# Kernel optimization log

Hardware: AMD Instinct MI355X
Metric: run time of the kernel (lower is better)

The kernel has to match this reference:

```python
import jax, jax.numpy as jnp
import numpy as np

B, S, D_IN, D_H, D_OUT = 4, 2048, 512, 512, 512


def setup_inputs() -> dict:
    key = jax.random.key(0)
    ks = jax.random.split(key, 11)
    s_in = 1.0 / np.sqrt(D_IN)
    s_cat = 1.0 / np.sqrt(3 * D_H)
    return {
        "x1": jax.random.normal(ks[0], (B, S, D_IN), jnp.float32),
        "x2": jax.random.normal(ks[1], (B, S, D_IN), jnp.float32),
        "x3": jax.random.normal(ks[2], (B, S, D_IN), jnp.float32),
        "Wq": jax.random.normal(ks[3], (D_IN, D_H), jnp.float32) * s_in,
        "bq": jnp.zeros((D_H,), jnp.float32),
        "Wk": jax.random.normal(ks[4], (D_IN, D_H), jnp.float32) * s_in,
        "bk": jnp.zeros((D_H,), jnp.float32),
        "Wv": jax.random.normal(ks[5], (D_IN, D_H), jnp.float32) * s_in,
        "bv": jnp.zeros((D_H,), jnp.float32),
        "Wo": jax.random.normal(ks[6], (3 * D_H, D_OUT), jnp.float32) * s_cat,
        "bo": jnp.zeros((D_OUT,), jnp.float32),
    }


def _attn(Q, K, V):
    # Q: [B,S,H], K/V: [B,S,H] -> [B,S,H]
    scale = 1.0 / jnp.sqrt(jnp.asarray(K.shape[-1], Q.dtype))
    scores = jnp.einsum('bqh,bkh->bqk', Q, K) * scale
    w = jax.nn.softmax(scores, axis=-1)
    return jnp.einsum('bqk,bkh->bqh', w, V)


def reference(x1, x2, x3, Wq, bq, Wk, bk, Wv, bv, Wo, bo):
    Q1, Q2, Q3 = x1 @ Wq + bq, x2 @ Wq + bq, x3 @ Wq + bq
    K1, K2, K3 = x1 @ Wk + bk, x2 @ Wk + bk, x3 @ Wk + bk
    V1, V2, V3 = x1 @ Wv + bv, x2 @ Wv + bv, x3 @ Wv + bv
    fused_x1 = _attn(Q1, K2, V2) + _attn(Q1, K3, V3)
    fused_x2 = _attn(Q2, K1, V1) + _attn(Q2, K3, V3)
    fused_x3 = _attn(Q3, K1, V1) + _attn(Q3, K2, V2)
    fused = jnp.concatenate([fused_x1, fused_x2, fused_x3], axis=-1)
    return fused @ Wo + bo
```

## Files before the change

kernel.cpp:

```cpp
#include <hip/hip_runtime.h>
#include <hip/hip_bf16.h>

typedef __attribute__((ext_vector_type(4))) float  f32x4;
typedef __attribute__((ext_vector_type(8))) short  short8;
typedef __attribute__((ext_vector_type(4))) short  short4v;

#define GAS(p) ((const __attribute__((address_space(1))) void*)(p))
#define LAS(p) ((__attribute__((address_space(3))) void*)(p))

__device__ inline short bf16_of(float f) {
    union { float f; unsigned u; } v; v.f = f;
    unsigned r = v.u + 0x7FFFu + ((v.u >> 16) & 1u);
    return (short)(r >> 16);
}
__device__ inline float f_of_bf16(short h) {
    union { unsigned u; float f; } v; v.u = ((unsigned)(unsigned short)h) << 16;
    return v.f;
}

__device__ __forceinline__ void stage_tiles(const short* A, long lda,
                                            const short* B, long ldb,
                                            short* AsB, short* BsB) {
    const int tid = threadIdx.x;
    const int w = tid >> 6, l = tid & 63;
    const int r = l >> 2, ce = (l & 3) * 8;
#pragma unroll
    for (int q = 0; q < 2; ++q) {
        const int row = q * 64 + w * 16;
        __builtin_amdgcn_global_load_lds(GAS(A + (long)(row + r) * lda + ce),
                                         LAS(AsB + row * 32), 16, 0, 0);
        __builtin_amdgcn_global_load_lds(GAS(B + (long)(row + r) * ldb + ce),
                                         LAS(BsB + row * 32), 16, 0, 0);
    }
}

__device__ __forceinline__ void gemm_core(const short* A, long lda,
                                          const short* B, long ldb, int nk,
                                          short (*As)[4096], short (*Bs)[4096],
                                          f32x4 acc[4][4]) {
    const int tid = threadIdx.x;
    const int lane = tid & 63, wid = tid >> 6;
    const int wr = wid >> 1, wc = wid & 1;
    const int fr = lane & 15, fk = lane >> 4;
    const int ao = (wr * 64 + fr) * 32 + fk * 8;
    const int bo = (wc * 64 + fr) * 32 + fk * 8;

    stage_tiles(A, lda, B, ldb, As[0], Bs[0]);
    __syncthreads();
    for (int ks = 0; ks < nk; ++ks) {
        const int cur = ks & 1;
        if (ks + 1 < nk)
            stage_tiles(A + (ks + 1) * 32, lda, B + (ks + 1) * 32, ldb,
                        As[cur ^ 1], Bs[cur ^ 1]);
        short8 af[4], bf[4];
#pragma unroll
        for (int mi = 0; mi < 4; ++mi) af[mi] = *(const short8*)&As[cur][ao + mi * 512];
#pragma unroll
        for (int ni = 0; ni < 4; ++ni) bf[ni] = *(const short8*)&Bs[cur][bo + ni * 512];
#pragma unroll
        for (int mi = 0; mi < 4; ++mi)
#pragma unroll
            for (int ni = 0; ni < 4; ++ni)
                acc[mi][ni] = __builtin_amdgcn_mfma_f32_16x16x32_bf16(af[mi], bf[ni], acc[mi][ni], 0, 0, 0);
        __syncthreads();
    }
}

template<int BIAS, bool F32OUT>
__global__ __launch_bounds__(256, 2)
void gemm_bias(const short* __restrict__ A, long lda, const short* __restrict__ B, long ldb,
               void* __restrict__ Cp, long ldc, const float* __restrict__ bias, int nk) {
    __shared__ short As[2][4096], Bs[2][4096];
    const short* Ab = A + (long)blockIdx.x * 128 * lda;
    const short* Bb = B + (long)blockIdx.y * 128 * ldb;
    f32x4 acc[4][4] = {};
    gemm_core(Ab, lda, Bb, ldb, nk, As, Bs, acc);

    const int lane = threadIdx.x & 63, wid = threadIdx.x >> 6;
    const int wr = wid >> 1, wc = wid & 1, fr = lane & 15, fk = lane >> 4;
    const long r0 = (long)blockIdx.x * 128 + wr * 64 + fk * 4;
    const long c0 = (long)blockIdx.y * 128 + wc * 64 + fr;
#pragma unroll
    for (int mi = 0; mi < 4; ++mi)
#pragma unroll
        for (int ni = 0; ni < 4; ++ni) {
            const long rr = r0 + mi * 16, cc = c0 + ni * 16;
#pragma unroll
            for (int r = 0; r < 4; ++r) {
                float v = acc[mi][ni][r];
                if (BIAS == 1) v += bias[cc];
                if (BIAS == 2) v += bias[rr + r];
                if (F32OUT) ((float*)Cp)[(rr + r) * ldc + cc] = v;
                else        ((short*)Cp)[(rr + r) * ldc + cc] = bf16_of(v);
            }
        }
}

struct QKOff { long q[3], k[3], s[3], l[3]; };

__global__ __launch_bounds__(256, 2)
void qk_exp(const short* __restrict__ Q, const short* __restrict__ K,
            short* __restrict__ Sc, float* __restrict__ L, QKOff o, float kscale) {
    __shared__ short As[2][4096], Bs[2][4096];
    const int p = blockIdx.z >> 2, b = blockIdx.z & 3;
    const short* Ab = Q + o.q[p] + ((long)b * 2048 + (long)blockIdx.x * 128) * 512;
    const short* Bb = K + o.k[p] + ((long)b * 2048 + (long)blockIdx.y * 128) * 512;
    f32x4 acc[4][4] = {};
    gemm_core(Ab, 512, Bb, 512, 16, As, Bs, acc);

    short* Cb = Sc + o.s[p] + (long)b * 2048 * 2048;
    float* lb = L + o.l[p] + (long)b * 2048;
    const int lane = threadIdx.x & 63, wid = threadIdx.x >> 6;
    const int wr = wid >> 1, wc = wid & 1, fr = lane & 15, fk = lane >> 4;
    const int r0 = blockIdx.x * 128 + wr * 64 + fk * 4;
    const int c0 = blockIdx.y * 128 + wc * 64 + fr;

#pragma unroll
    for (int mi = 0; mi < 4; ++mi)
#pragma unroll
        for (int ni = 0; ni < 4; ++ni)
#pragma unroll
            for (int r = 0; r < 4; ++r)
                acc[mi][ni][r] = exp2f(acc[mi][ni][r] * kscale);

#pragma unroll
    for (int mi = 0; mi < 4; ++mi)
#pragma unroll
        for (int r = 0; r < 4; ++r) {
            float s = acc[mi][0][r] + acc[mi][1][r] + acc[mi][2][r] + acc[mi][3][r];
            s += __shfl_xor(s, 1); s += __shfl_xor(s, 2);
            s += __shfl_xor(s, 4); s += __shfl_xor(s, 8);
            if (fr == 0) atomicAdd(&lb[r0 + mi * 16 + r], s);
        }

#pragma unroll
    for (int mi = 0; mi < 4; ++mi)
#pragma unroll
        for (int ni = 0; ni < 4; ++ni)
#pragma unroll
            for (int r = 0; r < 4; ++r)
                Cb[(long)(r0 + mi * 16 + r) * 2048 + (c0 + ni * 16)] = bf16_of(acc[mi][ni][r]);
}

struct PVOff { long s[3], v[3], c[3], l[3]; int accf[3]; };

__global__ __launch_bounds__(256, 2)
void pv_div(const short* __restrict__ Sc, const short* __restrict__ VT,
            short* __restrict__ F, const float* __restrict__ L, PVOff o) {
    __shared__ short As[2][4096], Bs[2][4096];
    const int p = blockIdx.z >> 2, b = blockIdx.z & 3;
    const short* Ab = Sc + o.s[p] + ((long)b * 2048 + (long)blockIdx.x * 128) * 2048;
    const short* Bb = VT + o.v[p] + (long)b * 2048 + (long)blockIdx.y * 128 * 24576;
    f32x4 acc[4][4] = {};
    gemm_core(Ab, 2048, Bb, 24576, 64, As, Bs, acc);

    const int lane = threadIdx.x & 63, wid = threadIdx.x >> 6;
    const int wr = wid >> 1, wc = wid & 1, fr = lane & 15, fk = lane >> 4;
    const int r0loc = blockIdx.x * 128 + wr * 64 + fk * 4;
    const long rg0 = (long)b * 2048 + r0loc;
    const int c0 = blockIdx.y * 128 + wc * 64 + fr;
    const float* lb = L + o.l[p] + (long)b * 2048;
    short* Cb = F + o.c[p];

    float linv[4][4];
#pragma unroll
    for (int mi = 0; mi < 4; ++mi)
#pragma unroll
        for (int r = 0; r < 4; ++r) linv[mi][r] = 1.0f / lb[r0loc + mi * 16 + r];

    const int af = o.accf[p];
#pragma unroll
    for (int mi = 0; mi < 4; ++mi)
#pragma unroll
        for (int ni = 0; ni < 4; ++ni)
#pragma unroll
            for (int r = 0; r < 4; ++r) {
                const long idx = (rg0 + mi * 16 + r) * 1536 + (c0 + ni * 16);
                float v = acc[mi][ni][r] * linv[mi][r];
                if (af) v += f_of_bf16(Cb[idx]);
                Cb[idx] = bf16_of(v);
            }
}

__global__ __launch_bounds__(256)
void xconv(const float* __restrict__ x0, const float* __restrict__ x1,
           const float* __restrict__ x2, short* __restrict__ xb) {
    const float* s = blockIdx.z == 0 ? x0 : (blockIdx.z == 1 ? x1 : x2);
    const long i = ((long)blockIdx.x * 256 + threadIdx.x) * 8;
    f32x4 a = *(const f32x4*)(s + i), c = *(const f32x4*)(s + i + 4);
    short8 v;
    v[0] = bf16_of(a.x); v[1] = bf16_of(a.y); v[2] = bf16_of(a.z); v[3] = bf16_of(a.w);
    v[4] = bf16_of(c.x); v[5] = bf16_of(c.y); v[6] = bf16_of(c.z); v[7] = bf16_of(c.w);
    *(short8*)(xb + (long)blockIdx.z * 8192 * 512 + i) = v;
}

__global__ __launch_bounds__(256)
void transpose_to_bf16(const float* __restrict__ src, short* __restrict__ dst,
                       int rows, int cols) {
    __shared__ float t[32][33];
    const int lx = threadIdx.x & 31, ly = threadIdx.x >> 5;
    const int r0 = blockIdx.x * 32, c0 = blockIdx.y * 32;
#pragma unroll
    for (int p = 0; p < 4; ++p)
        t[ly + 8 * p][lx] = src[(long)(r0 + ly + 8 * p) * cols + (c0 + lx)];
    __syncthreads();
#pragma unroll
    for (int p = 0; p < 4; ++p)
        dst[(long)(c0 + ly + 8 * p) * rows + (r0 + lx)] = bf16_of(t[lx][ly + 8 * p]);
}

#define LDP 40
template<bool F32> struct StageRegs;
template<> struct StageRegs<true>  { f32x4 v[4]; };
template<> struct StageRegs<false> { short8 v[2]; };

template<bool F32>
__device__ inline void stage_load(const void* base, long ld, int tid, StageRegs<F32>& r) {
    if constexpr (F32) {
        const float* p = (const float*)base;
        const int row = tid >> 3, c = (tid & 7) * 4;
#pragma unroll
        for (int i = 0; i < 4; ++i)
            r.v[i] = *(const f32x4*)(p + (long)(row + 32 * i) * ld + c);
    } else {
        const short* p = (const short*)base;
        const int row = tid >> 2, c = (tid & 3) * 8;
#pragma unroll
        for (int i = 0; i < 2; ++i)
            r.v[i] = *(const short8*)(p + (long)(row + 64 * i) * ld + c);
    }
}
template<bool F32>
__device__ inline void stage_commit(short* lds, int tid, const StageRegs<F32>& r) {
    if constexpr (F32) {
        const int row = tid >> 3, c = (tid & 7) * 4;
#pragma unroll
        for (int i = 0; i < 4; ++i) {
            short4v h;
            h.x = bf16_of(r.v[i].x); h.y = bf16_of(r.v[i].y);
            h.z = bf16_of(r.v[i].z); h.w = bf16_of(r.v[i].w);
            *(short4v*)&lds[(row + 32 * i) * LDP + c] = h;
        }
    } else {
        const int row = tid >> 2, c = (tid & 3) * 8;
#pragma unroll
        for (int i = 0; i < 2; ++i)
            *(short8*)&lds[(row + 64 * i) * LDP + c] = r.v[i];
    }
}

template<bool AF32, bool BF32, int BIAS>
__global__ __launch_bounds__(256, 2)
void gemm_bt_f32(const void* __restrict__ Ap, const void* __restrict__ Bp,
                 short* __restrict__ Cp, const float* __restrict__ bias,
                 int K, long lda, long ldb, long ldc) {
    __shared__ short As[2][128 * LDP];
    __shared__ short Bs[2][128 * LDP];
    const int tid = threadIdx.x;
    const char* A = (const char*)Ap + (long)blockIdx.x * 128 * lda * (AF32 ? 4 : 2);
    const char* B = (const char*)Bp + (long)blockIdx.y * 128 * ldb * (BF32 ? 4 : 2);

    StageRegs<AF32> ra; StageRegs<BF32> rb;
    stage_load<AF32>(A, lda, tid, ra);
    stage_load<BF32>(B, ldb, tid, rb);
    stage_commit<AF32>(As[0], tid, ra);
    stage_commit<BF32>(Bs[0], tid, rb);
    __syncthreads();

    f32x4 acc[4][4] = {};
    const int lane = tid & 63, wid = tid >> 6;
    const int wr = wid >> 1, wc = wid & 1;
    const int fr = lane & 15, fk = lane >> 4;
    const int aoff = (wr * 64 + fr) * LDP + fk * 8;
    const int boff = (wc * 64 + fr) * LDP + fk * 8;

    const int nk = K / 32;
    for (int ks = 0; ks < nk; ++ks) {
        const int cur = ks & 1;
        if (ks + 1 < nk) {
            stage_load<AF32>(A + (long)(ks + 1) * 32 * (AF32 ? 4 : 2), lda, tid, ra);
            stage_load<BF32>(B + (long)(ks + 1) * 32 * (BF32 ? 4 : 2), ldb, tid, rb);
        }
        short8 af[4], bfr[4];
#pragma unroll
        for (int mi = 0; mi < 4; ++mi) af[mi] = *(const short8*)&As[cur][aoff + mi * 16 * LDP];
#pragma unroll
        for (int ni = 0; ni < 4; ++ni) bfr[ni] = *(const short8*)&Bs[cur][boff + ni * 16 * LDP];
#pragma unroll
        for (int mi = 0; mi < 4; ++mi)
#pragma unroll
            for (int ni = 0; ni < 4; ++ni)
                acc[mi][ni] = __builtin_amdgcn_mfma_f32_16x16x32_bf16(af[mi], bfr[ni], acc[mi][ni], 0, 0, 0);
        if (ks + 1 < nk) {
            stage_commit<AF32>(As[cur ^ 1], tid, ra);
            stage_commit<BF32>(Bs[cur ^ 1], tid, rb);
        }
        __syncthreads();
    }

    const long crow0 = (long)blockIdx.x * 128 + wr * 64 + fk * 4;
    const long ccol0 = (long)blockIdx.y * 128 + wc * 64 + fr;
#pragma unroll
    for (int mi = 0; mi < 4; ++mi)
#pragma unroll
        for (int ni = 0; ni < 4; ++ni) {
            const long rr = crow0 + mi * 16, cc = ccol0 + ni * 16;
#pragma unroll
            for (int r = 0; r < 4; ++r) {
                float v = acc[mi][ni][r];
                if (BIAS == 1) v += bias[cc];
                if (BIAS == 2) v += bias[rr + r];
                Cp[(rr + r) * ldc + cc] = bf16_of(v);
            }
        }
}

extern "C" void kernel_launch(void* const* d_in, const int* in_sizes, int n_in,
                              void* d_out, int out_size, void* d_ws, size_t ws_size,
                              hipStream_t stream) {
    const float* x[3] = { (const float*)d_in[0], (const float*)d_in[1], (const float*)d_in[2] };
    const float* Wq = (const float*)d_in[3]; const float* bq = (const float*)d_in[4];
    const float* Wk = (const float*)d_in[5]; const float* bk = (const float*)d_in[6];
    const float* Wv = (const float*)d_in[7]; const float* bv = (const float*)d_in[8];
    const float* Wo = (const float*)d_in[9]; const float* bo = (const float*)d_in[10];

    const long TOK = 8192;
    const long T3 = 3 * TOK;

    char* ws = (char*)d_ws;
    size_t off = 0;
    auto alloc = [&](size_t bytes) -> void* {
        void* pp = ws + off;
        off += (bytes + 255) & ~(size_t)255;
        return pp;
    };

    short* WqT = (short*)alloc(512L * 512 * 2);
    short* WkT = (short*)alloc(512L * 512 * 2);
    short* WvT = (short*)alloc(512L * 512 * 2);
    short* WoT = (short*)alloc(512L * 1536 * 2);
    short* Qb  = (short*)alloc(T3 * 512 * 2);
    short* Kb  = (short*)alloc(T3 * 512 * 2);
    short* VT  = (short*)alloc(512L * T3 * 2);
    short* fused = (short*)alloc(TOK * 1536 * 2);
    float* l   = (float*)alloc(6L * 4 * 2048 * 4);

    const size_t base = off;
    const size_t SCB = 4L * 2048 * 2048 * 2;
    const size_t XB  = T3 * 512 * 2;

    int nlive; bool use_xb;
    if      (ws_size >= base + XB + 3 * SCB) { nlive = 3; use_xb = true;  }
    else if (ws_size >= base + XB + SCB)     { nlive = 1; use_xb = true;  }
    else                                     { nlive = 1; use_xb = false; }
    short* xb     = use_xb ? (short*)alloc(XB) : nullptr;
    short* scores = (short*)alloc((size_t)nlive * SCB);

    const dim3 tb(256);

    hipMemsetAsync(l, 0, 6L * 4 * 2048 * 4, stream);

    transpose_to_bf16<<<dim3(16, 16), tb, 0, stream>>>(Wq, WqT, 512, 512);
    transpose_to_bf16<<<dim3(16, 16), tb, 0, stream>>>(Wk, WkT, 512, 512);
    transpose_to_bf16<<<dim3(16, 16), tb, 0, stream>>>(Wv, WvT, 512, 512);
    transpose_to_bf16<<<dim3(48, 16), tb, 0, stream>>>(Wo, WoT, 1536, 512);

    if (use_xb) {
        xconv<<<dim3(2048, 1, 3), tb, 0, stream>>>(x[0], x[1], x[2], xb);
        gemm_bias<1, false><<<dim3(192, 4), tb, 0, stream>>>(xb, 512, WqT, 512, Qb, 512, bq, 16);
        gemm_bias<1, false><<<dim3(192, 4), tb, 0, stream>>>(xb, 512, WkT, 512, Kb, 512, bk, 16);
        gemm_bias<2, false><<<dim3(4, 192), tb, 0, stream>>>(WvT, 512, xb, 512, VT, T3, bv, 16);
    } else {
        for (int i = 0; i < 3; ++i) {
            gemm_bt_f32<true, false, 1><<<dim3(64, 4), tb, 0, stream>>>(
                x[i], WqT, Qb + (long)i * TOK * 512, bq, 512, 512, 512, 512);
            gemm_bt_f32<true, false, 1><<<dim3(64, 4), tb, 0, stream>>>(
                x[i], WkT, Kb + (long)i * TOK * 512, bk, 512, 512, 512, 512);
            gemm_bt_f32<false, true, 2><<<dim3(4, 64), tb, 0, stream>>>(
                WvT, x[i], VT + (long)i * TOK, bv, 512, 512, 512, T3);
        }
    }

    const int imap[6] = {0, 1, 2, 0, 1, 2};
    const int jmap[6] = {1, 0, 0, 2, 2, 1};
    const int accf[6] = {0, 0, 0, 1, 1, 1};
    const float kscale = 0.04419417382415922f * 1.4426950408889634f;

    for (int g = 0; g < 6; g += nlive) {
        QKOff qo{}; PVOff po{};
        for (int pl = 0; pl < nlive; ++pl) {
            const int gp = g + pl;
            qo.q[pl] = (long)imap[gp] * TOK * 512;
            qo.k[pl] = (long)jmap[gp] * TOK * 512;
            qo.s[pl] = (long)pl * 4 * 2048 * 2048;
            qo.l[pl] = (long)gp * 4 * 2048;
            po.s[pl] = qo.s[pl];
            po.v[pl] = (long)jmap[gp] * TOK;
            po.c[pl] = (long)imap[gp] * 512;
            po.l[pl] = qo.l[pl];
            po.accf[pl] = accf[gp];
        }
        qk_exp<<<dim3(16, 16, 4 * nlive), tb, 0, stream>>>(Qb, Kb, scores, l, qo, kscale);
        pv_div<<<dim3(16, 4, 4 * nlive), tb, 0, stream>>>(scores, VT, fused, l, po);
    }

    gemm_bias<1, true><<<dim3(64, 4), tb, 0, stream>>>(fused, 1536, WoT, 1536, d_out, 512, bo, 48);
}
```

Measured before the change: 460.4 us.

## Use K=64 swizzled LDS tiles, LDS-bounced stores, deterministic row sums, split fused output

The GEMM core now stages 64-wide K tiles into XOR-swizzled LDS, which halves the number of loop iterations and barriers and avoids bank conflicts. Epilogues write bf16 results through an LDS bounce buffer so global stores are 16-byte coalesced. Softmax row sums move from atomics to per-block partials followed by a small reduction kernel. The second attention term goes to a separate fused buffer, so the read-modify-write in pv_div is gone and the sum happens in the output GEMM instead. This costs more workspace, an extra output GEMM pass, and doubled LDS per block, which may hurt occupancy.

```diff
diff --git a/kernel.cpp b/kernel.cpp
--- a/kernel.cpp
+++ b/kernel.cpp
@@ -3,7 +3,6 @@
 
 typedef __attribute__((ext_vector_type(4))) float  f32x4;
 typedef __attribute__((ext_vector_type(8))) short  short8;
-typedef __attribute__((ext_vector_type(4))) short  short4v;
 
 #define GAS(p) ((const __attribute__((address_space(1))) void*)(p))
 #define LAS(p) ((__attribute__((address_space(3))) void*)(p))
@@ -18,63 +17,126 @@
     return v.f;
 }
 
-__device__ __forceinline__ void stage_tiles(const short* A, long lda,
-                                            const short* B, long ldb,
-                                            short* AsB, short* BsB) {
+__device__ __forceinline__ void stage64(const short* A, long lda,
+                                        const short* B, long ldb,
+                                        short* As, short* Bs) {
     const int tid = threadIdx.x;
     const int w = tid >> 6, l = tid & 63;
-    const int r = l >> 2, ce = (l & 3) * 8;
-#pragma unroll
-    for (int q = 0; q < 2; ++q) {
-        const int row = q * 64 + w * 16;
-        __builtin_amdgcn_global_load_lds(GAS(A + (long)(row + r) * lda + ce),
-                                         LAS(AsB + row * 32), 16, 0, 0);
-        __builtin_amdgcn_global_load_lds(GAS(B + (long)(row + r) * ldb + ce),
-                                         LAS(BsB + row * 32), 16, 0, 0);
-    }
-}
-
-__device__ __forceinline__ void gemm_core(const short* A, long lda,
-                                          const short* B, long ldb, int nk,
-                                          short (*As)[4096], short (*Bs)[4096],
-                                          f32x4 acc[4][4]) {
+    const int r = l >> 3;
+    const int scol = ((l & 7) ^ r) * 8;
+#pragma unroll
+    for (int q = 0; q < 4; ++q) {
+        const int rowb = q * 32 + w * 8;
+        __builtin_amdgcn_global_load_lds(GAS(A + (long)(rowb + r) * lda + scol),
+                                         LAS(As + rowb * 64), 16, 0, 0);
+        __builtin_amdgcn_global_load_lds(GAS(B + (long)(rowb + r) * ldb + scol),
+                                         LAS(Bs + rowb * 64), 16, 0, 0);
+    }
+}
+
+__device__ __forceinline__ void gemm_core64(const short* A, long lda,
+                                            const short* B, long ldb, int nk,
+                                            short* sA, short* sB,
+                                            f32x4 acc[4][4]) {
     const int tid = threadIdx.x;
     const int lane = tid & 63, wid = tid >> 6;
     const int wr = wid >> 1, wc = wid & 1;
     const int fr = lane & 15, fk = lane >> 4;
-    const int ao = (wr * 64 + fr) * 32 + fk * 8;
-    const int bo = (wc * 64 + fr) * 32 + fk * 8;
-
-    stage_tiles(A, lda, B, ldb, As[0], Bs[0]);
+    const int swz = (fr & 7) << 4;
+    const int abase = (wr * 64 + fr) * 128 + fk * 16;
+    const int bbase = (wc * 64 + fr) * 128 + fk * 16;
+
+    stage64(A, lda, B, ldb, sA, sB);
     __syncthreads();
     for (int ks = 0; ks < nk; ++ks) {
         const int cur = ks & 1;
         if (ks + 1 < nk)
-            stage_tiles(A + (ks + 1) * 32, lda, B + (ks + 1) * 32, ldb,
-                        As[cur ^ 1], Bs[cur ^ 1]);
-        short8 af[4], bf[4];
-#pragma unroll
-        for (int mi = 0; mi < 4; ++mi) af[mi] = *(const short8*)&As[cur][ao + mi * 512];
-#pragma unroll
-        for (int ni = 0; ni < 4; ++ni) bf[ni] = *(const short8*)&Bs[cur][bo + ni * 512];
-#pragma unroll
-        for (int mi = 0; mi < 4; ++mi)
+            stage64(A + (ks + 1) * 64, lda, B + (ks + 1) * 64, ldb,
+                    sA + (cur ^ 1) * 8192, sB + (cur ^ 1) * 8192);
+        const char* pa = (const char*)(sA + cur * 8192);
+        const char* pb = (const char*)(sB + cur * 8192);
+        short8 af[2][4], bf[2][4];
+#pragma unroll
+        for (int kk = 0; kk < 2; ++kk) {
+#pragma unroll
+            for (int mi = 0; mi < 4; ++mi)
+                af[kk][mi] = *(const short8*)(pa + (((abase + kk * 64) ^ swz) + mi * 2048));
 #pragma unroll
             for (int ni = 0; ni < 4; ++ni)
-                acc[mi][ni] = __builtin_amdgcn_mfma_f32_16x16x32_bf16(af[mi], bf[ni], acc[mi][ni], 0, 0, 0);
+                bf[kk][ni] = *(const short8*)(pb + (((bbase + kk * 64) ^ swz) + ni * 2048));
+        }
+#pragma unroll
+        for (int kk = 0; kk < 2; ++kk)
+#pragma unroll
+            for (int mi = 0; mi < 4; ++mi)
+#pragma unroll
+                for (int ni = 0; ni < 4; ++ni)
+                    acc[mi][ni] = __builtin_amdgcn_mfma_f32_16x16x32_bf16(af[kk][mi], bf[kk][ni], acc[mi][ni], 0, 0, 0);
         __syncthreads();
     }
 }
 
-template<int BIAS, bool F32OUT>
+__device__ __forceinline__ void bounce_store(short* Pb, const short vals[4][4][4],
+                                             short* C, long ldc) {
+    const int tid = threadIdx.x, lane = tid & 63, wid = tid >> 6;
+    const int wr = wid >> 1, wc = wid & 1, fr = lane & 15, fk = lane >> 4;
+#pragma unroll
+    for (int mi = 0; mi < 4; ++mi)
+#pragma unroll
+        for (int ni = 0; ni < 4; ++ni)
+#pragma unroll
+            for (int r = 0; r < 4; ++r) {
+                const int row = wr * 64 + mi * 16 + fk * 4 + r;
+                const int col = wc * 64 + ni * 16 + fr;
+                Pb[row * 128 + (col ^ ((row & 7) << 3))] = vals[mi][ni][r];
+            }
+    __syncthreads();
+#pragma unroll
+    for (int i = 0; i < 8; ++i) {
+        const int row = i * 16 + (tid >> 4);
+        const int ch = tid & 15;
+        short8 v = *(const short8*)&Pb[row * 128 + ((ch * 8) ^ ((row & 7) << 3))];
+        *(short8*)&C[(long)row * ldc + ch * 8] = v;
+    }
+}
+
+template<int BIAS>
 __global__ __launch_bounds__(256, 2)
-void gemm_bias(const short* __restrict__ A, long lda, const short* __restrict__ B, long ldb,
-               void* __restrict__ Cp, long ldc, const float* __restrict__ bias, int nk) {
-    __shared__ short As[2][4096], Bs[2][4096];
+void gemm_bias16(const short* __restrict__ A, long lda, const short* __restrict__ B, long ldb,
+                 short* __restrict__ C, long ldc, const float* __restrict__ bias, int nk) {
+    __shared__ short sA[2 * 8192], sB[2 * 8192];
     const short* Ab = A + (long)blockIdx.x * 128 * lda;
     const short* Bb = B + (long)blockIdx.y * 128 * ldb;
     f32x4 acc[4][4] = {};
-    gemm_core(Ab, lda, Bb, ldb, nk, As, Bs, acc);
+    gemm_core64(Ab, lda, Bb, ldb, nk, sA, sB, acc);
+
+    const int lane = threadIdx.x & 63, wid = threadIdx.x >> 6;
+    const int wr = wid >> 1, wc = wid & 1, fr = lane & 15, fk = lane >> 4;
+    const long r0 = (long)blockIdx.x * 128, c0 = (long)blockIdx.y * 128;
+    short vals[4][4][4];
+#pragma unroll
+    for (int mi = 0; mi < 4; ++mi)
+#pragma unroll
+        for (int ni = 0; ni < 4; ++ni)
+#pragma unroll
+            for (int r = 0; r < 4; ++r) {
+                float v = acc[mi][ni][r];
+                if (BIAS == 1) v += bias[c0 + wc * 64 + ni * 16 + fr];
+                if (BIAS == 2) v += bias[r0 + wr * 64 + mi * 16 + fk * 4 + r];
+                vals[mi][ni][r] = bf16_of(v);
+            }
+    bounce_store(sA, vals, C + r0 * ldc + c0, ldc);
+}
+
+template<bool ACC>
+__global__ __launch_bounds__(256, 2)
+void gemm_f32(const short* __restrict__ A, long lda, const short* __restrict__ B, long ldb,
+              float* __restrict__ C, long ldc, const float* __restrict__ bias, int nk) {
+    __shared__ short sA[2 * 8192], sB[2 * 8192];
+    const short* Ab = A + (long)blockIdx.x * 128 * lda;
+    const short* Bb = B + (long)blockIdx.y * 128 * ldb;
+    f32x4 acc[4][4] = {};
+    gemm_core64(Ab, lda, Bb, ldb, nk, sA, sB, acc);
 
     const int lane = threadIdx.x & 63, wid = threadIdx.x >> 6;
     const int wr = wid >> 1, wc = wid & 1, fr = lane & 15, fk = lane >> 4;
@@ -88,32 +150,30 @@
 #pragma unroll
             for (int r = 0; r < 4; ++r) {
                 float v = acc[mi][ni][r];
-                if (BIAS == 1) v += bias[cc];
-                if (BIAS == 2) v += bias[rr + r];
-                if (F32OUT) ((float*)Cp)[(rr + r) * ldc + cc] = v;
-                else        ((short*)Cp)[(rr + r) * ldc + cc] = bf16_of(v);
+                if (!ACC) v += bias[cc];
+                const long idx = (rr + r) * ldc + cc;
+                if (ACC) v += C[idx];
+                C[idx] = v;
             }
         }
 }
 
-struct QKOff { long q[3], k[3], s[3], l[3]; };
+struct Off6 { long a[6], b[6]; };
 
 __global__ __launch_bounds__(256, 2)
 void qk_exp(const short* __restrict__ Q, const short* __restrict__ K,
-            short* __restrict__ Sc, float* __restrict__ L, QKOff o, float kscale) {
-    __shared__ short As[2][4096], Bs[2][4096];
-    const int p = blockIdx.z >> 2, b = blockIdx.z & 3;
-    const short* Ab = Q + o.q[p] + ((long)b * 2048 + (long)blockIdx.x * 128) * 512;
-    const short* Bb = K + o.k[p] + ((long)b * 2048 + (long)blockIdx.y * 128) * 512;
+            short* __restrict__ Sc, float* __restrict__ lpart,
+            Off6 o, int z0, float kscale) {
+    __shared__ short sA[2 * 8192], sB[2 * 8192];
+    const int slice = z0 + blockIdx.z;
+    const int gp = slice >> 2, b = slice & 3;
+    const short* Ab = Q + o.a[gp] + ((long)b * 2048 + (long)blockIdx.x * 128) * 512;
+    const short* Bb = K + o.b[gp] + ((long)b * 2048 + (long)blockIdx.y * 128) * 512;
     f32x4 acc[4][4] = {};
-    gemm_core(Ab, 512, Bb, 512, 16, As, Bs, acc);
-
-    short* Cb = Sc + o.s[p] + (long)b * 2048 * 2048;
-    float* lb = L + o.l[p] + (long)b * 2048;
-    const int lane = threadIdx.x & 63, wid = threadIdx.x >> 6;
-    const int wr = wid >> 1, wc = wid & 1, fr = lane & 15, fk = lane >> 4;
-    const int r0 = blockIdx.x * 128 + wr * 64 + fk * 4;
-    const int c0 = blockIdx.y * 128 + wc * 64 + fr;
+    gemm_core64(Ab, 512, Bb, 512, 8, sA, sB, acc);
+
+    const int tid = threadIdx.x, lane = tid & 63, wid = tid >> 6;
+    const int wr = wid >> 1, wc = wid & 1, fr = lane & 15, fk = lane >> 4;
 
 #pragma unroll
     for (int mi = 0; mi < 4; ++mi)
@@ -130,56 +190,72 @@
             float s = acc[mi][0][r] + acc[mi][1][r] + acc[mi][2][r] + acc[mi][3][r];
             s += __shfl_xor(s, 1); s += __shfl_xor(s, 2);
             s += __shfl_xor(s, 4); s += __shfl_xor(s, 8);
-            if (fr == 0) atomicAdd(&lb[r0 + mi * 16 + r], s);
+            if (fr == 0)
+                lpart[((long)slice * 32 + blockIdx.y * 2 + wc) * 2048 +
+                      (long)blockIdx.x * 128 + wr * 64 + mi * 16 + fk * 4 + r] = s;
         }
 
+    short vals[4][4][4];
 #pragma unroll
     for (int mi = 0; mi < 4; ++mi)
 #pragma unroll
         for (int ni = 0; ni < 4; ++ni)
 #pragma unroll
             for (int r = 0; r < 4; ++r)
-                Cb[(long)(r0 + mi * 16 + r) * 2048 + (c0 + ni * 16)] = bf16_of(acc[mi][ni][r]);
-}
-
-struct PVOff { long s[3], v[3], c[3], l[3]; int accf[3]; };
+                vals[mi][ni][r] = bf16_of(acc[mi][ni][r]);
+
+    short* Cb = Sc + (long)blockIdx.z * 2048 * 2048 +
+                (long)blockIdx.x * 128 * 2048 + (long)blockIdx.y * 128;
+    bounce_store(sA, vals, Cb, 2048);
+}
+
+__global__ __launch_bounds__(256)
+void lred(const float* __restrict__ lpart, float* __restrict__ l, int z0) {
+    const int slice = z0 + (blockIdx.x >> 3);
+    const int row = (blockIdx.x & 7) * 256 + threadIdx.x;
+    float s = 0.f;
+#pragma unroll
+    for (int j = 0; j < 32; ++j)
+        s += lpart[((long)slice * 32 + j) * 2048 + row];
+    l[(long)slice * 2048 + row] = s;
+}
+
+struct POff { long v[6], c[6]; int f2[6]; };
 
 __global__ __launch_bounds__(256, 2)
 void pv_div(const short* __restrict__ Sc, const short* __restrict__ VT,
-            short* __restrict__ F, const float* __restrict__ L, PVOff o) {
-    __shared__ short As[2][4096], Bs[2][4096];
-    const int p = blockIdx.z >> 2, b = blockIdx.z & 3;
-    const short* Ab = Sc + o.s[p] + ((long)b * 2048 + (long)blockIdx.x * 128) * 2048;
-    const short* Bb = VT + o.v[p] + (long)b * 2048 + (long)blockIdx.y * 128 * 24576;
+            const float* __restrict__ l, short* __restrict__ F1,
+            short* __restrict__ F2, POff o, int z0) {
+    __shared__ short sA[2 * 8192], sB[2 * 8192];
+    const int slice = z0 + blockIdx.z;
+    const int gp = slice >> 2, b = slice & 3;
+    const short* Ab = Sc + (long)blockIdx.z * 2048 * 2048 + (long)blockIdx.x * 128 * 2048;
+    const short* Bb = VT + o.v[gp] + (long)b * 2048 + (long)blockIdx.y * 128 * 24576;
     f32x4 acc[4][4] = {};
-    gemm_core(Ab, 2048, Bb, 24576, 64, As, Bs, acc);
-
-    const int lane = threadIdx.x & 63, wid = threadIdx.x >> 6;
-    const int wr = wid >> 1, wc = wid & 1, fr = lane & 15, fk = lane >> 4;
-    const int r0loc = blockIdx.x * 128 + wr * 64 + fk * 4;
-    const long rg0 = (long)b * 2048 + r0loc;
-    const int c0 = blockIdx.y * 128 + wc * 64 + fr;
-    const float* lb = L + o.l[p] + (long)b * 2048;
-    short* Cb = F + o.c[p];
-
-    float linv[4][4];
-#pragma unroll
-    for (int mi = 0; mi < 4; ++mi)
-#pragma unroll
-        for (int r = 0; r < 4; ++r) linv[mi][r] = 1.0f / lb[r0loc + mi * 16 + r];
-
-    const int af = o.accf[p];
-#pragma unroll
-    for (int mi = 0; mi < 4; ++mi)
-#pragma unroll
-        for (int ni = 0; ni < 4; ++ni)
-#pragma unroll
-            for (int r = 0; r < 4; ++r) {
-                const long idx = (rg0 + mi * 16 + r) * 1536 + (c0 + ni * 16);
-                float v = acc[mi][ni][r] * linv[mi][r];
-                if (af) v += f_of_bf16(Cb[idx]);
-                Cb[idx] = bf16_of(v);
-            }
+    gemm_core64(Ab, 2048, Bb, 24576, 32, sA, sB, acc);
+
+    const int tid = threadIdx.x, lane = tid & 63, wid = tid >> 6;
+    const int wr = wid >> 1, wc = wid & 1, fr = lane & 15, fk = lane >> 4;
+    const float* lb = l + (long)slice * 2048 + (long)blockIdx.x * 128;
+
+    short vals[4][4][4];
+#pragma unroll
+    for (int mi = 0; mi < 4; ++mi) {
+        float linv[4];
+#pragma unroll
+        for (int r = 0; r < 4; ++r)
+            linv[r] = 1.0f / lb[wr * 64 + mi * 16 + fk * 4 + r];
+#pragma unroll
+        for (int ni = 0; ni < 4; ++ni)
+#pragma unroll
+            for (int r = 0; r < 4; ++r)
+                vals[mi][ni][r] = bf16_of(acc[mi][ni][r] * linv[r]);
+    }
+
+    short* F = (o.f2[gp] ? F2 : F1);
+    short* Cb = F + ((long)b * 2048 + (long)blockIdx.x * 128) * 1536 +
+                o.c[gp] + (long)blockIdx.y * 128;
+    bounce_store(sA, vals, Cb, 1536);
 }
 
 __global__ __launch_bounds__(256)
@@ -209,112 +285,6 @@
         dst[(long)(c0 + ly + 8 * p) * rows + (r0 + lx)] = bf16_of(t[lx][ly + 8 * p]);
 }
 
-#define LDP 40
-template<bool F32> struct StageRegs;
-template<> struct StageRegs<true>  { f32x4 v[4]; };
-template<> struct StageRegs<false> { short8 v[2]; };
-
-template<bool F32>
-__device__ inline void stage_load(const void* base, long ld, int tid, StageRegs<F32>& r) {
-    if constexpr (F32) {
-        const float* p = (const float*)base;
-        const int row = tid >> 3, c = (tid & 7) * 4;
-#pragma unroll
-        for (int i = 0; i < 4; ++i)
-            r.v[i] = *(const f32x4*)(p + (long)(row + 32 * i) * ld + c);
-    } else {
-        const short* p = (const short*)base;
-        const int row = tid >> 2, c = (tid & 3) * 8;
-#pragma unroll
-        for (int i = 0; i < 2; ++i)
-            r.v[i] = *(const short8*)(p + (long)(row + 64 * i) * ld + c);
-    }
-}
-template<bool F32>
-__device__ inline void stage_commit(short* lds, int tid, const StageRegs<F32>& r) {
-    if constexpr (F32) {
-        const int row = tid >> 3, c = (tid & 7) * 4;
-#pragma unroll
-        for (int i = 0; i < 4; ++i) {
-            short4v h;
-            h.x = bf16_of(r.v[i].x); h.y = bf16_of(r.v[i].y);
-            h.z = bf16_of(r.v[i].z); h.w = bf16_of(r.v[i].w);
-            *(short4v*)&lds[(row + 32 * i) * LDP + c] = h;
-        }
-    } else {
-        const int row = tid >> 2, c = (tid & 3) * 8;
-#pragma unroll
-        for (int i = 0; i < 2; ++i)
-            *(short8*)&lds[(row + 64 * i) * LDP + c] = r.v[i];
-    }
-}
-
-template<bool AF32, bool BF32, int BIAS>
-__global__ __launch_bounds__(256, 2)
-void gemm_bt_f32(const void* __restrict__ Ap, const void* __restrict__ Bp,
-                 short* __restrict__ Cp, const float* __restrict__ bias,
-                 int K, long lda, long ldb, long ldc) {
-    __shared__ short As[2][128 * LDP];
-    __shared__ short Bs[2][128 * LDP];
-    const int tid = threadIdx.x;
-    const char* A = (const char*)Ap + (long)blockIdx.x * 128 * lda * (AF32 ? 4 : 2);
-    const char* B = (const char*)Bp + (long)blockIdx.y * 128 * ldb * (BF32 ? 4 : 2);
-
-    StageRegs<AF32> ra; StageRegs<BF32> rb;
-    stage_load<AF32>(A, lda, tid, ra);
-    stage_load<BF32>(B, ldb, tid, rb);
-    stage_commit<AF32>(As[0], tid, ra);
-    stage_commit<BF32>(Bs[0], tid, rb);
-    __syncthreads();
-
-    f32x4 acc[4][4] = {};
-    const int lane = tid & 63, wid = tid >> 6;
-    const int wr = wid >> 1, wc = wid & 1;
-    const int fr = lane & 15, fk = lane >> 4;
-    const int aoff = (wr * 64 + fr) * LDP + fk * 8;
-    const int boff = (wc * 64 + fr) * LDP + fk * 8;
-
-    const int nk = K / 32;
-    for (int ks = 0; ks < nk; ++ks) {
-        const int cur = ks & 1;
-        if (ks + 1 < nk) {
-            stage_load<AF32>(A + (long)(ks + 1) * 32 * (AF32 ? 4 : 2), lda, tid, ra);
-            stage_load<BF32>(B + (long)(ks + 1) * 32 * (BF32 ? 4 : 2), ldb, tid, rb);
-        }
-        short8 af[4], bfr[4];
-#pragma unroll
-        for (int mi = 0; mi < 4; ++mi) af[mi] = *(const short8*)&As[cur][aoff + mi * 16 * LDP];
-#pragma unroll
-        for (int ni = 0; ni < 4; ++ni) bfr[ni] = *(const short8*)&Bs[cur][boff + ni * 16 * LDP];
-#pragma unroll
-        for (int mi = 0; mi < 4; ++mi)
-#pragma unroll
-            for (int ni = 0; ni < 4; ++ni)
-                acc[mi][ni] = __builtin_amdgcn_mfma_f32_16x16x32_bf16(af[mi], bfr[ni], acc[mi][ni], 0, 0, 0);
-        if (ks + 1 < nk) {
-            stage_commit<AF32>(As[cur ^ 1], tid, ra);
-            stage_commit<BF32>(Bs[cur ^ 1], tid, rb);
-        }
-        __syncthreads();
-    }
-
-    const long crow0 = (long)blockIdx.x * 128 + wr * 64 + fk * 4;
-    const long ccol0 = (long)blockIdx.y * 128 + wc * 64 + fr;
-#pragma unroll
-    for (int mi = 0; mi < 4; ++mi)
-#pragma unroll
-        for (int ni = 0; ni < 4; ++ni) {
-            const long rr = crow0 + mi * 16, cc = ccol0 + ni * 16;
-#pragma unroll
-            for (int r = 0; r < 4; ++r) {
-                float v = acc[mi][ni][r];
-                if (BIAS == 1) v += bias[cc];
-                if (BIAS == 2) v += bias[rr + r];
-                Cp[(rr + r) * ldc + cc] = bf16_of(v);
-            }
-        }
-}
-
 extern "C" void kernel_launch(void* const* d_in, const int* in_sizes, int n_in,
                               void* d_out, int out_size, void* d_ws, size_t ws_size,
                               hipStream_t stream) {
@@ -324,8 +294,7 @@
     const float* Wv = (const float*)d_in[7]; const float* bv = (const float*)d_in[8];
     const float* Wo = (const float*)d_in[9]; const float* bo = (const float*)d_in[10];
 
-    const long TOK = 8192;
-    const long T3 = 3 * TOK;
+    const long TOK = 8192, T3 = 3 * TOK;
 
     char* ws = (char*)d_ws;
     size_t off = 0;
@@ -342,67 +311,48 @@
     short* Qb  = (short*)alloc(T3 * 512 * 2);
     short* Kb  = (short*)alloc(T3 * 512 * 2);
     short* VT  = (short*)alloc(512L * T3 * 2);
-    short* fused = (short*)alloc(TOK * 1536 * 2);
-    float* l   = (float*)alloc(6L * 4 * 2048 * 4);
-
-    const size_t base = off;
-    const size_t SCB = 4L * 2048 * 2048 * 2;
-    const size_t XB  = T3 * 512 * 2;
-
-    int nlive; bool use_xb;
-    if      (ws_size >= base + XB + 3 * SCB) { nlive = 3; use_xb = true;  }
-    else if (ws_size >= base + XB + SCB)     { nlive = 1; use_xb = true;  }
-    else                                     { nlive = 1; use_xb = false; }
-    short* xb     = use_xb ? (short*)alloc(XB) : nullptr;
-    short* scores = (short*)alloc((size_t)nlive * SCB);
+    short* fused1 = (short*)alloc(TOK * 1536 * 2);
+    short* fused2 = (short*)alloc(TOK * 1536 * 2);
+    float* l    = (float*)alloc(24L * 2048 * 4);
+    float* lpart = (float*)alloc(24L * 32 * 2048 * 4);
+    short* xb   = (short*)alloc(T3 * 512 * 2);
+
+    const size_t SLICE = 2048L * 2048 * 2;
+    int nsl;
+    if      (ws_size >= off + 24 * SLICE) nsl = 24;
+    else if (ws_size >= off + 12 * SLICE) nsl = 12;
+    else                                  nsl = 4;
+    short* scores = (short*)alloc((size_t)nsl * SLICE);
 
     const dim3 tb(256);
-
-    hipMemsetAsync(l, 0, 6L * 4 * 2048 * 4, stream);
-
     transpose_to_bf16<<<dim3(16, 16), tb, 0, stream>>>(Wq, WqT, 512, 512);
     transpose_to_bf16<<<dim3(16, 16), tb, 0, stream>>>(Wk, WkT, 512, 512);
     transpose_to_bf16<<<dim3(16, 16), tb, 0, stream>>>(Wv, WvT, 512, 512);
     transpose_to_bf16<<<dim3(48, 16), tb, 0, stream>>>(Wo, WoT, 1536, 512);
-
-    if (use_xb) {
-        xconv<<<dim3(2048, 1, 3), tb, 0, stream>>>(x[0], x[1], x[2], xb);
-        gemm_bias<1, false><<<dim3(192, 4), tb, 0, stream>>>(xb, 512, WqT, 512, Qb, 512, bq, 16);
-        gemm_bias<1, false><<<dim3(192, 4), tb, 0, stream>>>(xb, 512, WkT, 512, Kb, 512, bk, 16);
-        gemm_bias<2, false><<<dim3(4, 192), tb, 0, stream>>>(WvT, 512, xb, 512, VT, T3, bv, 16);
-    } else {
-        for (int i = 0; i < 3; ++i) {
-            gemm_bt_f32<true, false, 1><<<dim3(64, 4), tb, 0, stream>>>(
-                x[i], WqT, Qb + (long)i * TOK * 512, bq, 512, 512, 512, 512);
-            gemm_bt_f32<true, false, 1><<<dim3(64, 4), tb, 0, stream>>>(
-                x[i], WkT, Kb + (long)i * TOK * 512, bk, 512, 512, 512, 512);
-            gemm_bt_f32<false, true, 2><<<dim3(4, 64), tb, 0, stream>>>(
-                WvT, x[i], VT + (long)i * TOK, bv, 512, 512, 512, T3);
-        }
-    }
+    xconv<<<dim3(2048, 1, 3), tb, 0, stream>>>(x[0], x[1], x[2], xb);
+
+    gemm_bias16<1><<<dim3(192, 4), tb, 0, stream>>>(xb, 512, WqT, 512, Qb, 512, bq, 8);
+    gemm_bias16<1><<<dim3(192, 4), tb, 0, stream>>>(xb, 512, WkT, 512, Kb, 512, bk, 8);
+    gemm_bias16<2><<<dim3(4, 192), tb, 0, stream>>>(WvT, 512, xb, 512, VT, T3, bv, 8);
 
     const int imap[6] = {0, 1, 2, 0, 1, 2};
     const int jmap[6] = {1, 0, 0, 2, 2, 1};
-    const int accf[6] = {0, 0, 0, 1, 1, 1};
+    Off6 qo{}; POff po{};
+    for (int gp = 0; gp < 6; ++gp) {
+        qo.a[gp] = (long)imap[gp] * TOK * 512;
+        qo.b[gp] = (long)jmap[gp] * TOK * 512;
+        po.v[gp] = (long)jmap[gp] * TOK;
+        po.c[gp] = (long)imap[gp] * 512;
+        po.f2[gp] = (gp >= 3);
+    }
     const float kscale = 0.04419417382415922f * 1.4426950408889634f;
 
-    for (int g = 0; g < 6; g += nlive) {
-        QKOff qo{}; PVOff po{};
-        for (int pl = 0; pl < nlive; ++pl) {
-            const int gp = g + pl;
-            qo.q[pl] = (long)imap[gp] * TOK * 512;
-            qo.k[pl] = (long)jmap[gp] * TOK * 512;
-            qo.s[pl] = (long)pl * 4 * 2048 * 2048;
-            qo.l[pl] = (long)gp * 4 * 2048;
-            po.s[pl] = qo.s[pl];
-            po.v[pl] = (long)jmap[gp] * TOK;
-            po.c[pl] = (long)imap[gp] * 512;
-            po.l[pl] = qo.l[pl];
-            po.accf[pl] = accf[gp];
-        }
-        qk_exp<<<dim3(16, 16, 4 * nlive), tb, 0, stream>>>(Qb, Kb, scores, l, qo, kscale);
-        pv_div<<<dim3(16, 4, 4 * nlive), tb, 0, stream>>>(scores, VT, fused, l, po);
-    }
-
-    gemm_bias<1, true><<<dim3(64, 4), tb, 0, stream>>>(fused, 1536, WoT, 1536, d_out, 512, bo, 48);
-}
+    for (int z0 = 0; z0 < 24; z0 += nsl) {
+        qk_exp<<<dim3(16, 16, nsl), tb, 0, stream>>>(Qb, Kb, scores, lpart, qo, z0, kscale);
+        lred<<<dim3(nsl * 8), tb, 0, stream>>>(lpart, l, z0);
+        pv_div<<<dim3(16, 4, nsl), tb, 0, stream>>>(scores, VT, l, fused1, fused2, po, z0);
+    }
+
+    gemm_f32<false><<<dim3(64, 4), tb, 0, stream>>>(fused1, 1536, WoT, 1536, (float*)d_out, 512, bo, 24);
+    gemm_f32<true><<<dim3(64, 4), tb, 0, stream>>>(fused2, 1536, WoT, 1536, (float*)d_out, 512, nullptr, 24);
+}
```

New measurement: 502.7 us. 1.09x slower.
